# Optimization experiments

Hardware: AMD Instinct MI355X
Metric: run time of the kernel (lower is better)

Reference implementation:

```python
import jax, jax.numpy as jnp
import numpy as np

B, T, D, SD, CHUNK = 4, 4096, 1024, 512, 32


def setup_inputs() -> dict:
    key = jax.random.key(0)
    ks = jax.random.split(key, 6)
    sc_in = 1.0 / np.sqrt(D)
    sc_out = 1.0 / np.sqrt(2 * SD)
    return {
        "x": jax.random.normal(ks[0], (B, T, D), jnp.float32),
        "Wt": jax.random.normal(ks[1], (D, SD), jnp.float32) * sc_in,
        "bt": jnp.zeros((SD,), jnp.float32),
        "Wr": jax.random.normal(ks[2], (D, SD), jnp.float32) * sc_in,
        "br": jnp.zeros((SD,), jnp.float32),
        "Wi": jax.random.normal(ks[3], (D, 2 * SD), jnp.float32) * sc_in,
        "bi": jnp.zeros((2 * SD,), jnp.float32),
        "Wo": jax.random.normal(ks[4], (2 * SD, D), jnp.float32) * sc_out,
        "bo": jnp.zeros((D,), jnp.float32),
        "gamma": jnp.ones((D,), jnp.float32),
        "beta": jnp.zeros((D,), jnp.float32),
    }


def _rotation_scan(theta, retain, b_r, b_i, chunk):
    # theta/retain/b_*: [B, T, d]. Chunked linear recurrence h[t]=a[t]*h[t-1]+b[t]
    # with a[t] = retain[t]*e^{i theta[t]}, done in log-magnitude/angle space.
    Bsz, Tlen, d = theta.shape
    K = min(chunk, Tlen)
    n = Tlen // K  # T assumed divisible by K (4096 / 32)
    resh = lambda a: a.reshape(Bsz, n, K, d).transpose(1, 0, 2, 3)  # [n,B,K,d]
    th_c, rt_c, br_c, bi_c = resh(theta), resh(retain), resh(b_r), resh(b_i)

    def step(carry, xs):
        h_r, h_i = carry  # [B, d]
        th, rt, cb_r, cb_i = xs  # [B, K, d]
        cum_log_mag = jnp.cumsum(jnp.log(jnp.clip(rt, 1e-6, None)), axis=1)
        cum_mag = jnp.exp(cum_log_mag)
        cum_th = jnp.cumsum(th, axis=1)
        cum_cos = jnp.cos(cum_th)
        cum_sin = jnp.sin(cum_th)
        cum_a_r = cum_mag * cum_cos
        cum_a_i = cum_mag * cum_sin
        inv_mag = 1.0 / jnp.clip(cum_mag, 1e-8, None)
        inv_r = inv_mag * cum_cos          # cos(-t) = cos(t)
        inv_i = -inv_mag * cum_sin         # sin(-t) = -sin(t)
        scaled_b_r = inv_r * cb_r - inv_i * cb_i
        scaled_b_i = inv_r * cb_i + inv_i * cb_r
        cum_b_r = jnp.cumsum(scaled_b_r, axis=1)
        cum_b_i = jnp.cumsum(scaled_b_i, axis=1)
        tot_r = h_r[:, None] + cum_b_r
        tot_i = h_i[:, None] + cum_b_i
        ch_r = cum_a_r * tot_r - cum_a_i * tot_i
        ch_i = cum_a_r * tot_i + cum_a_i * tot_r
        return (ch_r[:, -1], ch_i[:, -1]), (ch_r, ch_i)

    h0 = (jnp.zeros((Bsz, d), theta.dtype), jnp.zeros((Bsz, d), theta.dtype))
    _, (out_r, out_i) = jax.lax.scan(step, h0, (th_c, rt_c, br_c, bi_c))
    back = lambda a: a.transpose(1, 0, 2, 3).reshape(Bsz, Tlen, d)
    return back(out_r), back(out_i)


def reference(x, Wt, bt, Wr, br, Wi, bi, Wo, bo, gamma, beta):
    d = Wt.shape[1]
    theta = x @ Wt + bt                       # [B,T,d]
    retain = jax.nn.sigmoid(x @ Wr + br)      # [B,T,d]
    inp = x @ Wi + bi                          # [B,T,2d]
    inp_r, inp_i = inp[..., :d], inp[..., d:]
    drive = 1.0 - retain
    out_r, out_i = _rotation_scan(theta, retain, drive * inp_r, drive * inp_i, CHUNK)
    out = jnp.concatenate([out_r, out_i], axis=-1)  # [B,T,2d]
    y = x + out @ Wo + bo
    mu = jnp.mean(y, axis=-1, keepdims=True)
    var = jnp.var(y, axis=-1, keepdims=True)
    return (y - mu) / jnp.sqrt(var + 1e-5) * gamma + beta
```

## Files before the change

kernel.cpp:

```cpp
#include <hip/hip_runtime.h>
#include <cstdint>


typedef __bf16 bf16x8 __attribute__((ext_vector_type(8)));
typedef float  f32x4  __attribute__((ext_vector_type(4)));
typedef ushort u16x8  __attribute__((ext_vector_type(8)));

#define AS1 __attribute__((address_space(1)))
#define AS3 __attribute__((address_space(3)))

__device__ __forceinline__ void gload16(const void* g, void* l) {
  __builtin_amdgcn_global_load_lds((const AS1 void*)g, (AS3 void*)l, 16, 0, 0);
}

__device__ __forceinline__ ushort f2bf(float f) {
  union { float f; uint32_t u; } v; v.f = f;
  uint32_t u = v.u;
  uint32_t r = u + 0x7FFFu + ((u >> 16) & 1u);
  return (ushort)(r >> 16);
}
__device__ __forceinline__ float bf2f(ushort u) {
  union { uint32_t x; float f; } v; v.x = (uint32_t)u << 16; return v.f;
}
__device__ __forceinline__ u16x8 cvt8(float4 a, float4 b) {
  u16x8 o;
  o[0] = f2bf(a.x); o[1] = f2bf(a.y); o[2] = f2bf(a.z); o[3] = f2bf(a.w);
  o[4] = f2bf(b.x); o[5] = f2bf(b.y); o[6] = f2bf(b.z); o[7] = f2bf(b.w);
  return o;
}

__global__ __launch_bounds__(256) void tconv_all(const float* __restrict__ Wt,
                                                 const float* __restrict__ Wr,
                                                 const float* __restrict__ Wi,
                                                 const float* __restrict__ Wo,
                                                 ushort* __restrict__ wcat,
                                                 ushort* __restrict__ wot) {
  const int z = blockIdx.z;
  if (z < 2 && blockIdx.x >= 16) return;
  const float* src = (z == 0) ? Wt : (z == 1) ? Wr : (z == 2) ? Wi : Wo;
  const int C = (z < 2) ? 512 : 1024;
  const int row_off = (z == 0) ? 0 : (z == 1) ? 512 : (z == 2) ? 1024 : 0;
  ushort* dst = (z == 3) ? wot : wcat;

  __shared__ float tile[32][33];
  int tx = threadIdx.x, ty = threadIdx.y;
  int rb = blockIdx.y * 32, cb = blockIdx.x * 32;
#pragma unroll
  for (int yy = 0; yy < 4; ++yy) {
    int r = rb + ty + yy * 8;
    tile[ty + yy * 8][tx] = src[(size_t)r * C + cb + tx];
  }
  __syncthreads();
#pragma unroll
  for (int yy = 0; yy < 4; ++yy) {
    int c = cb + ty + yy * 8;
    dst[(size_t)(row_off + c) * 1024 + rb + tx] = f2bf(tile[tx][ty + yy * 8]);
  }
}

__global__ __launch_bounds__(256) void pack_bias(const float* __restrict__ bt,
                                                 const float* __restrict__ br,
                                                 const float* __restrict__ bi,
                                                 float* __restrict__ bcat) {
  int i = blockIdx.x * 256 + threadIdx.x;
  bcat[i] = (i < 512) ? bt[i] : (i < 1024 ? br[i - 512] : bi[i - 1024]);
}

template <bool AF32>
__global__ __launch_bounds__(512, 2) void gemm256(const void* __restrict__ Aptr,
                                                  const ushort* __restrict__ Bt,
                                                  ushort* __restrict__ C,
                                                  const float* __restrict__ bias,
                                                  int M, int N, int K, int nbn) {
  __shared__ alignas(16) ushort smem[65536];
  ushort* const As0 = smem;
  ushort* const Bs0 = smem + 2 * 256 * 64;

  const int cpx = gridDim.x >> 3;
  const int wg = ((int)blockIdx.x & 7) * cpx + ((int)blockIdx.x >> 3);
  const int bm = wg / nbn, bn = wg % nbn;

  const int t = threadIdx.x;
  const int l = t & 63, w = t >> 6;
  const int wm = w >> 2, wn = w & 3;
  const int r = l & 15, kq = l >> 4;

  const size_t a0 = (size_t)bm * 256 * K;
  const size_t b0 = (size_t)bn * 256 * K;

  const int srow = t >> 3;
  const int sslot = (t & 7) ^ (srow & 7);
  const ushort* gA16 = (const ushort*)Aptr + a0 + (size_t)srow * K + sslot * 8;
  const float*  gAf  = (const float*)Aptr + a0 + (size_t)srow * K + sslot * 8;
  const ushort* gB = Bt + b0 + (size_t)srow * K + sslot * 8;
  const int lboff = w * 1024 + l * 16;

  f32x4 acc[8][4] = {};
  const int NKT = K >> 6;
  float4 areg[4][2];

#define STGA(buf, kt, u) \
  gload16(gA16 + (size_t)((u) * 64) * K + (size_t)(kt) * 64, \
          (char*)(As0 + (buf) * 256 * 64) + (u) * 8192 + lboff)
#define STGB(buf, kt, u) \
  gload16(gB + (size_t)((u) * 64) * K + (size_t)(kt) * 64, \
          (char*)(Bs0 + (buf) * 256 * 64) + (u) * 8192 + lboff)
#define ALOAD(kt, u) \
  do { const float* gs_ = gAf + (size_t)((u) * 64) * K + (size_t)(kt) * 64; \
       areg[u][0] = *(const float4*)gs_; areg[u][1] = *(const float4*)(gs_ + 4); } while (0)
#define AWRITE(buf, u) \
  *(u16x8*)((char*)(As0 + (buf) * 256 * 64) + (u) * 8192 + lboff) = cvt8(areg[u][0], areg[u][1])

#define QUAD(ph)                                                               \
  do {                                                                         \
    _Pragma("unroll")                                                          \
    for (int ii = 0; ii < 2; ++ii) {                                           \
      bf16x8 aF[2];                                                            \
      const int rowa = wm * 128 + ((ph) * 2 + ii) * 16 + r;                    \
      _Pragma("unroll")                                                        \
      for (int ks = 0; ks < 2; ++ks) {                                         \
        const int j = (ks * 4 + kq) ^ (r & 7);                                 \
        aF[ks] = *(const bf16x8*)&pA[rowa * 64 + j * 8];                       \
      }                                                                        \
      __builtin_amdgcn_s_setprio(1);                                           \
      _Pragma("unroll")                                                        \
      for (int jn = 0; jn < 4; ++jn)                                           \
        _Pragma("unroll")                                                      \
        for (int ks = 0; ks < 2; ++ks)                                         \
          acc[(ph) * 2 + ii][jn] = __builtin_amdgcn_mfma_f32_16x16x32_bf16(    \
              aF[ks], bF[jn][ks], acc[(ph) * 2 + ii][jn], 0, 0, 0);            \
      __builtin_amdgcn_s_setprio(0);                                           \
    }                                                                          \
  } while (0)

  if constexpr (AF32) {
#pragma unroll
    for (int u = 0; u < 4; ++u) ALOAD(0, u);
    STGB(0, 0, 0); STGB(0, 0, 1); STGB(0, 0, 2); STGB(0, 0, 3);
#pragma unroll
    for (int u = 0; u < 4; ++u) AWRITE(0, u);
    if (NKT > 1) {
#pragma unroll
      for (int u = 0; u < 4; ++u) ALOAD(1, u);
    }
  } else {
    STGB(0, 0, 0); STGB(0, 0, 1); STGB(0, 0, 2); STGB(0, 0, 3);
    STGA(0, 0, 0); STGA(0, 0, 2); STGA(0, 0, 1); STGA(0, 0, 3);
  }

  for (int kt = 0; kt < NKT; ++kt) {
    const int cur = kt & 1, nxt = cur ^ 1;
    const bool hn = (kt + 1 < NKT);
    const ushort* pA = As0 + cur * 256 * 64;
    const ushort* pB = Bs0 + cur * 256 * 64;

    if (hn) { STGB(nxt, kt + 1, 0); STGB(nxt, kt + 1, 1); }
    if constexpr (AF32) {
      if (hn) asm volatile("s_waitcnt vmcnt(10) lgkmcnt(0)" ::: "memory");
      else    asm volatile("s_waitcnt vmcnt(0) lgkmcnt(0)" ::: "memory");
    } else {
      if (hn) asm volatile("s_waitcnt vmcnt(2)" ::: "memory");
      else    asm volatile("s_waitcnt vmcnt(0)" ::: "memory");
    }
    __builtin_amdgcn_s_barrier();
    asm volatile("" ::: "memory");
    bf16x8 bF[4][2];
#pragma unroll
    for (int jn = 0; jn < 4; ++jn) {
      const int rowb = wn * 64 + jn * 16 + r;
#pragma unroll
      for (int ks = 0; ks < 2; ++ks) {
        const int j = (ks * 4 + kq) ^ (r & 7);
        bF[jn][ks] = *(const bf16x8*)&pB[rowb * 64 + j * 8];
      }
    }
    QUAD(0);
    if (hn) { STGB(nxt, kt + 1, 2); STGB(nxt, kt + 1, 3); }
    QUAD(1);
    bf16x8 aFn[2][2];
#pragma unroll
    for (int ii = 0; ii < 2; ++ii) {
      const int rowa = wm * 128 + (4 + ii) * 16 + r;
#pragma unroll
      for (int ks = 0; ks < 2; ++ks) {
        const int j = (ks * 4 + kq) ^ (r & 7);
        aFn[ii][ks] = *(const bf16x8*)&pA[rowa * 64 + j * 8];
      }
    }
    if constexpr (AF32) {
      if (hn) { AWRITE(nxt, 0); AWRITE(nxt, 1); }
      if (kt + 2 < NKT) { ALOAD(kt + 2, 0); ALOAD(kt + 2, 1); }
    } else {
      if (hn) { STGA(nxt, kt + 1, 0); STGA(nxt, kt + 1, 2); }
    }
    asm volatile("" ::: "memory");
    __builtin_amdgcn_s_barrier();
    __builtin_amdgcn_s_setprio(1);
#pragma unroll
    for (int ii = 0; ii < 2; ++ii)
#pragma unroll
      for (int jn = 0; jn < 4; ++jn)
#pragma unroll
        for (int ks = 0; ks < 2; ++ks)
          acc[4 + ii][jn] = __builtin_amdgcn_mfma_f32_16x16x32_bf16(
              aFn[ii][ks], bF[jn][ks], acc[4 + ii][jn], 0, 0, 0);
    __builtin_amdgcn_s_setprio(0);
    if constexpr (AF32) {
      if (hn) { AWRITE(nxt, 2); AWRITE(nxt, 3); }
      if (kt + 2 < NKT) { ALOAD(kt + 2, 2); ALOAD(kt + 2, 3); }
    } else {
      if (hn) { STGA(nxt, kt + 1, 1); STGA(nxt, kt + 1, 3); }
    }
    QUAD(3);
  }
#undef STGA
#undef STGB
#undef ALOAD
#undef AWRITE
#undef QUAD

  asm volatile("s_waitcnt lgkmcnt(0) vmcnt(0)" ::: "memory");
  __builtin_amdgcn_s_barrier();

  const int q4 = (l >> 4) * 4;
  float bvj[4];
#pragma unroll
  for (int jn = 0; jn < 4; ++jn) {
    const int col = wn * 64 + jn * 16 + r;
    bvj[jn] = bias ? bias[bn * 256 + col] : 0.f;
  }
#pragma unroll
  for (int i = 0; i < 8; ++i) {
#pragma unroll
    for (int jn = 0; jn < 4; ++jn) {
      const int col = wn * 64 + jn * 16 + r;
      const int chunk = col >> 3;
#pragma unroll
      for (int q = 0; q < 4; ++q) {
        const int rowl = wm * 128 + i * 16 + q4 + q;
        const int pch = chunk ^ (rowl & 7);
        smem[rowl * 256 + pch * 8 + (col & 7)] = f2bf(acc[i][jn][q] + bvj[jn]);
      }
    }
  }
  __builtin_amdgcn_s_barrier();

  const int rrow0 = t >> 5;
  const int rch = t & 31;
#pragma unroll
  for (int p = 0; p < 16; ++p) {
    const int rowl = p * 16 + rrow0;
    const int pch = rch ^ (rowl & 7);
    u16x8 vv = *(const u16x8*)&smem[rowl * 256 + pch * 8];
    const size_t grow = (size_t)(bm * 256 + rowl);
    *(u16x8*)&C[grow * N + bn * 256 + rch * 8] = vv;
  }
}

__global__ __launch_bounds__(256) void scan_k1(const ushort* __restrict__ lin,
                                               float4* __restrict__ agg) {
  int bd = blockIdx.x * 256 + threadIdx.x;
  int c  = blockIdx.y;
  int b  = bd >> 9, d = bd & 511;
  const ushort* base = lin + ((size_t)b * 4096 + (size_t)c * 32) * 2048;
  float cth = 0.f, cbr = 0.f, cbi = 0.f;
  float cm = 1.f, cs = 1.f, sn = 0.f;
#pragma unroll 4
  for (int t = 0; t < 32; ++t) {
    const ushort* row = base + (size_t)t * 2048;
    float th = bf2f(row[d]);
    float z  = bf2f(row[512 + d]);
    float ir = bf2f(row[1024 + d]);
    float ii = bf2f(row[1536 + d]);
    float rt = __fdividef(1.f, 1.f + __expf(-z));
    cm *= fmaxf(rt, 1e-6f);
    cth += th;
    float s_, c_;
    __sincosf(cth, &s_, &c_);
    float im = __fdividef(1.f, fmaxf(cm, 1e-8f));
    float invr = im * c_, invi = -im * s_;
    float drive = 1.f - rt;
    float br_ = drive * ir, bi_ = drive * ii;
    cbr += invr * br_ - invi * bi_;
    cbi += invr * bi_ + invi * br_;
    cs = c_; sn = s_;
  }
  agg[(size_t)c * 2048 + bd] = make_float4(cm * cs, cm * sn, cbr, cbi);
}

__global__ __launch_bounds__(256) void scan_k2(const float4* __restrict__ agg,
                                               float2* __restrict__ h0) {
  int bd = blockIdx.x * 256 + threadIdx.x;
  float hr = 0.f, hi = 0.f;
  for (int cg = 0; cg < 16; ++cg) {
    float4 a[8];
#pragma unroll
    for (int u = 0; u < 8; ++u) a[u] = agg[(size_t)(cg * 8 + u) * 2048 + bd];
#pragma unroll
    for (int u = 0; u < 8; ++u) {
      h0[(size_t)(cg * 8 + u) * 2048 + bd] = make_float2(hr, hi);
      float tr = hr + a[u].z, ti = hi + a[u].w;
      hr = a[u].x * tr - a[u].y * ti;
      hi = a[u].x * ti + a[u].y * tr;
    }
  }
}

__global__ __launch_bounds__(256) void scan_k3(const ushort* __restrict__ lin,
                                               const float2* __restrict__ h0,
                                               ushort* __restrict__ outb) {
  int bd = blockIdx.x * 256 + threadIdx.x;
  int c  = blockIdx.y;
  int b  = bd >> 9, d = bd & 511;
  const ushort* base = lin + ((size_t)b * 4096 + (size_t)c * 32) * 2048;
  float2 h = h0[(size_t)c * 2048 + bd];
  float cth = 0.f, cbr = 0.f, cbi = 0.f, cm = 1.f;
#pragma unroll 4
  for (int t = 0; t < 32; ++t) {
    const ushort* row = base + (size_t)t * 2048;
    float th = bf2f(row[d]);
    float z  = bf2f(row[512 + d]);
    float ir = bf2f(row[1024 + d]);
    float ii = bf2f(row[1536 + d]);
    float rt = __fdividef(1.f, 1.f + __expf(-z));
    cm *= fmaxf(rt, 1e-6f);
    cth += th;
    float s_, c_;
    __sincosf(cth, &s_, &c_);
    float im = __fdividef(1.f, fmaxf(cm, 1e-8f));
    float invr = im * c_, invi = -im * s_;
    float drive = 1.f - rt;
    float br_ = drive * ir, bi_ = drive * ii;
    cbr += invr * br_ - invi * bi_;
    cbi += invr * bi_ + invi * br_;
    float ar = cm * c_, ai = cm * s_;
    float tr = h.x + cbr, ti = h.y + cbi;
    float orr = ar * tr - ai * ti;
    float oii = ar * ti + ai * tr;
    size_t rowo = ((size_t)b * 4096 + (size_t)c * 32 + t) * 1024;
    outb[rowo + d] = f2bf(orr);
    outb[rowo + 512 + d] = f2bf(oii);
  }
}

__global__ __launch_bounds__(256) void ln_k(const ushort* __restrict__ yb,
                                            const float* __restrict__ x,
                                            const float* __restrict__ gamma,
                                            const float* __restrict__ beta,
                                            float* __restrict__ out) {
  const int lane = threadIdx.x & 63;
  const size_t row = (size_t)blockIdx.x * 4 + (threadIdx.x >> 6);
  const ushort* yr = yb + row * 1024;
  const float* xr = x + row * 1024;
  float v[4][4];
  float s = 0.f, s2 = 0.f;
#pragma unroll
  for (int q = 0; q < 4; ++q) {
    ushort4 uy = *(const ushort4*)(yr + q * 256 + lane * 4);
    float4 fx = *(const float4*)(xr + q * 256 + lane * 4);
    v[q][0] = bf2f(uy.x) + fx.x;
    v[q][1] = bf2f(uy.y) + fx.y;
    v[q][2] = bf2f(uy.z) + fx.z;
    v[q][3] = bf2f(uy.w) + fx.w;
#pragma unroll
    for (int j = 0; j < 4; ++j) { s += v[q][j]; s2 += v[q][j] * v[q][j]; }
  }
#pragma unroll
  for (int off = 32; off > 0; off >>= 1) {
    s  += __shfl_xor(s, off);
    s2 += __shfl_xor(s2, off);
  }
  const float mu = s * (1.f / 1024.f);
  const float rstd = rsqrtf(s2 * (1.f / 1024.f) - mu * mu + 1e-5f);
#pragma unroll
  for (int q = 0; q < 4; ++q) {
    float4 gv = *(const float4*)(gamma + q * 256 + lane * 4);
    float4 bv = *(const float4*)(beta + q * 256 + lane * 4);
    float4 o;
    o.x = (v[q][0] - mu) * rstd * gv.x + bv.x;
    o.y = (v[q][1] - mu) * rstd * gv.y + bv.y;
    o.z = (v[q][2] - mu) * rstd * gv.z + bv.z;
    o.w = (v[q][3] - mu) * rstd * gv.w + bv.w;
    *(float4*)(out + row * 1024 + q * 256 + lane * 4) = o;
  }
}

extern "C" void kernel_launch(void* const* d_in, const int* in_sizes, int n_in,
                              void* d_out, int out_size, void* d_ws, size_t ws_size,
                              hipStream_t stream) {
  (void)in_sizes; (void)n_in; (void)out_size; (void)ws_size;
  const float* x  = (const float*)d_in[0];
  const float* Wt = (const float*)d_in[1];
  const float* bt = (const float*)d_in[2];
  const float* Wr = (const float*)d_in[3];
  const float* br = (const float*)d_in[4];
  const float* Wi = (const float*)d_in[5];
  const float* bi = (const float*)d_in[6];
  const float* Wo = (const float*)d_in[7];
  const float* bo = (const float*)d_in[8];
  const float* gamma = (const float*)d_in[9];
  const float* beta  = (const float*)d_in[10];

  char* ws = (char*)d_ws;
  ushort* wcat_t = (ushort*)(ws);
  ushort* wo_t   = (ushort*)(ws + ((size_t)4  << 20));
  float*  bcat   = (float*) (ws + ((size_t)6  << 20));
  float4* agg    = (float4*)(ws + ((size_t)8  << 20));
  float2* h0     = (float2*)(ws + ((size_t)12 << 20));
  ushort* outb   = (ushort*)(ws + ((size_t)48 << 20));
  ushort* linb   = (ushort*)(ws + ((size_t)80 << 20));
  ushort* yb     = (ushort*)(ws + ((size_t)80 << 20));

  tconv_all<<<dim3(32, 32, 4), dim3(32, 8), 0, stream>>>(Wt, Wr, Wi, Wo, wcat_t, wo_t);
  pack_bias<<<8, 256, 0, stream>>>(bt, br, bi, bcat);

  gemm256<true><<<512, 512, 0, stream>>>(x, wcat_t, linb, bcat, 16384, 2048, 1024, 8);

  scan_k1<<<dim3(8, 128), 256, 0, stream>>>(linb, agg);
  scan_k2<<<8, 256, 0, stream>>>(agg, h0);
  scan_k3<<<dim3(8, 128), 256, 0, stream>>>(linb, h0, outb);

  gemm256<false><<<256, 512, 0, stream>>>(outb, wo_t, yb, bo, 16384, 1024, 1024, 4);

  ln_k<<<4096, 256, 0, stream>>>(yb, x, gamma, beta, (float*)d_out);
}
```

Baseline: 193.4 us.

## Add 8-phase pipelined bf16 GEMM kernel for the output projection

Introduces a new gemm8p kernel for the output projection (bf16 A input). It splits each K-tile into four quarter phases, interleaving LDS fragment reads, async global-to-LDS loads of the next A tile and the tile-after-next B tile, barriers and MFMA groups. The aim is to overlap memory staging with matrix math more finely than gemm256<false>. The tighter schedule adds barriers per K-step and depends on careful vmcnt accounting for correctness.

```diff
diff --git a/kernel.cpp b/kernel.cpp
--- a/kernel.cpp
+++ b/kernel.cpp
@@ -218,6 +218,175 @@
 #undef ALOAD
 #undef AWRITE
 #undef QUAD
+
+  asm volatile("s_waitcnt lgkmcnt(0) vmcnt(0)" ::: "memory");
+  __builtin_amdgcn_s_barrier();
+
+  const int q4 = (l >> 4) * 4;
+  float bvj[4];
+#pragma unroll
+  for (int jn = 0; jn < 4; ++jn) {
+    const int col = wn * 64 + jn * 16 + r;
+    bvj[jn] = bias ? bias[bn * 256 + col] : 0.f;
+  }
+#pragma unroll
+  for (int i = 0; i < 8; ++i) {
+#pragma unroll
+    for (int jn = 0; jn < 4; ++jn) {
+      const int col = wn * 64 + jn * 16 + r;
+      const int chunk = col >> 3;
+#pragma unroll
+      for (int q = 0; q < 4; ++q) {
+        const int rowl = wm * 128 + i * 16 + q4 + q;
+        const int pch = chunk ^ (rowl & 7);
+        smem[rowl * 256 + pch * 8 + (col & 7)] = f2bf(acc[i][jn][q] + bvj[jn]);
+      }
+    }
+  }
+  __builtin_amdgcn_s_barrier();
+
+  const int rrow0 = t >> 5;
+  const int rch = t & 31;
+#pragma unroll
+  for (int p = 0; p < 16; ++p) {
+    const int rowl = p * 16 + rrow0;
+    const int pch = rch ^ (rowl & 7);
+    u16x8 vv = *(const u16x8*)&smem[rowl * 256 + pch * 8];
+    const size_t grow = (size_t)(bm * 256 + rowl);
+    *(u16x8*)&C[grow * N + bn * 256 + rch * 8] = vv;
+  }
+}
+
+__global__ __launch_bounds__(512, 2) void gemm8p(const ushort* __restrict__ A,
+                                                 const ushort* __restrict__ Bt,
+                                                 ushort* __restrict__ C,
+                                                 const float* __restrict__ bias,
+                                                 int M, int N, int K, int nbn) {
+  __shared__ alignas(16) ushort smem[65536];
+  char* const sm = (char*)smem;
+
+  const int cpx = gridDim.x >> 3;
+  const int wg = ((int)blockIdx.x & 7) * cpx + ((int)blockIdx.x >> 3);
+  const int bm = wg / nbn, bn = wg % nbn;
+
+  const int t = threadIdx.x;
+  const int l = t & 63, w = t >> 6;
+  const int wm = w >> 2, wn = w & 3;
+  const int r = l & 15, kq = l >> 4;
+  const int bh = wn >> 1;
+  const int lbrow0 = (wn & 1) * 64;
+
+  const size_t a0 = (size_t)bm * 256 * K;
+  const size_t b0 = (size_t)bn * 256 * K;
+
+  const int srow = t >> 3;
+  const int sslot = (t & 7) ^ (srow & 7);
+  const ushort* gA = A + a0 + (size_t)srow * K + sslot * 8;
+  const ushort* gB = Bt + b0 + (size_t)srow * K + sslot * 8;
+  const int lboff = w * 1024 + l * 16;
+
+  f32x4 acc[8][4] = {};
+  const int NKT = K >> 6;
+
+#define STG_A(buf, half, kt) do {                                              \
+    gload16(gA + (size_t)((half) * 128) * K + (size_t)(kt) * 64,               \
+            sm + ((buf) * 2 + (half)) * 16384 + lboff);                        \
+    gload16(gA + (size_t)((half) * 128 + 64) * K + (size_t)(kt) * 64,          \
+            sm + ((buf) * 2 + (half)) * 16384 + 8192 + lboff);                 \
+  } while (0)
+#define STG_B(buf, half, kt) do {                                              \
+    gload16(gB + (size_t)((half) * 128) * K + (size_t)(kt) * 64,               \
+            sm + 65536 + ((buf) * 2 + (half)) * 16384 + lboff);                \
+    gload16(gB + (size_t)((half) * 128 + 64) * K + (size_t)(kt) * 64,          \
+            sm + 65536 + ((buf) * 2 + (half)) * 16384 + 8192 + lboff);         \
+  } while (0)
+
+#define READQ(ph)                                                              \
+  { _Pragma("unroll")                                                          \
+    for (int ii = 0; ii < 2; ++ii) {                                           \
+      const int la = ((ph) * 2 + ii) * 16 + r;                                 \
+      _Pragma("unroll")                                                        \
+      for (int ks = 0; ks < 2; ++ks) {                                         \
+        const int j = (ks * 4 + kq) ^ (r & 7);                                 \
+        aF[ii][ks] = *(const bf16x8*)(pA + la * 64 + j * 8);                   \
+      }                                                                        \
+    } }
+
+#define MMAQ(ph)                                                               \
+  __builtin_amdgcn_s_setprio(1);                                               \
+  _Pragma("unroll")                                                            \
+  for (int ii = 0; ii < 2; ++ii)                                               \
+    _Pragma("unroll")                                                          \
+    for (int jn = 0; jn < 4; ++jn)                                             \
+      _Pragma("unroll")                                                        \
+      for (int ks = 0; ks < 2; ++ks)                                           \
+        acc[(ph) * 2 + ii][jn] = __builtin_amdgcn_mfma_f32_16x16x32_bf16(      \
+            aF[ii][ks], bF[jn][ks], acc[(ph) * 2 + ii][jn], 0, 0, 0);          \
+  __builtin_amdgcn_s_setprio(0);
+
+#define PH_SYNC                                                                \
+  asm volatile("" ::: "memory");                                               \
+  __builtin_amdgcn_s_barrier();                                                \
+  asm volatile("s_waitcnt lgkmcnt(0)" ::: "memory");
+
+#define PH_END                                                                 \
+  asm volatile("" ::: "memory");                                               \
+  __builtin_amdgcn_s_barrier();
+
+  STG_B(0, 0, 0); STG_B(0, 1, 0);
+  STG_A(0, 0, 0); STG_A(0, 1, 0);
+  STG_B(1, 0, 1); STG_B(1, 1, 1);
+  asm volatile("s_waitcnt vmcnt(4)" ::: "memory");
+  __builtin_amdgcn_s_barrier();
+
+  for (int kt = 0; kt < NKT; ++kt) {
+    const int cur = kt & 1, nxt = cur ^ 1;
+    const ushort* pA = (const ushort*)(sm + (cur * 2 + wm) * 16384);
+    const ushort* pB = (const ushort*)(sm + 65536 + (cur * 2 + bh) * 16384);
+    bf16x8 bF[4][2];
+    bf16x8 aF[2][2];
+
+#pragma unroll
+    for (int jn = 0; jn < 4; ++jn) {
+      const int rowb = lbrow0 + jn * 16 + r;
+#pragma unroll
+      for (int ks = 0; ks < 2; ++ks) {
+        const int j = (ks * 4 + kq) ^ (r & 7);
+        bF[jn][ks] = *(const bf16x8*)(pB + rowb * 64 + j * 8);
+      }
+    }
+    READQ(0);
+    if (kt + 1 < NKT) STG_A(nxt, 0, kt + 1);
+    PH_SYNC;
+    MMAQ(0);
+    PH_END;
+    READQ(1);
+    if (kt + 1 < NKT) STG_A(nxt, 1, kt + 1);
+    PH_SYNC;
+    MMAQ(1);
+    PH_END;
+    READQ(2);
+    if (kt + 2 < NKT) STG_B(cur, 0, kt + 2);
+    PH_SYNC;
+    MMAQ(2);
+    PH_END;
+    READQ(3);
+    if (kt + 2 < NKT) {
+      STG_B(cur, 1, kt + 2);
+      asm volatile("s_waitcnt vmcnt(4)" ::: "memory");
+    } else {
+      asm volatile("s_waitcnt vmcnt(0)" ::: "memory");
+    }
+    PH_SYNC;
+    MMAQ(3);
+    PH_END;
+  }
+#undef STG_A
+#undef STG_B
+#undef READQ
+#undef MMAQ
+#undef PH_SYNC
+#undef PH_END
 
   asm volatile("s_waitcnt lgkmcnt(0) vmcnt(0)" ::: "memory");
   __builtin_amdgcn_s_barrier();
@@ -420,7 +589,7 @@
   scan_k2<<<8, 256, 0, stream>>>(agg, h0);
   scan_k3<<<dim3(8, 128), 256, 0, stream>>>(linb, h0, outb);
 
-  gemm256<false><<<256, 512, 0, stream>>>(outb, wo_t, yb, bo, 16384, 1024, 1024, 4);
+  gemm8p<<<256, 512, 0, stream>>>(outb, wo_t, yb, bo, 16384, 1024, 1024, 4);
 
   ln_k<<<4096, 256, 0, stream>>>(yb, x, gamma, beta, (float*)d_out);
 }
```

Measured after the change: 194.9 us. Within noise of the previous version (+0.8%).
